# Kernel tuning notes

Measured on AMD Instinct MI355X. Metric: run time of the kernel, lower is better.

The kernel has to match this reference:

```python
import jax, jax.numpy as jnp
import numpy as np

N = 100000   # total nodes
E = 500000   # directed edges
G = 100      # graphs in batch (1000 nodes each)
D = 146      # in/hidden/out dim
C = 10       # classes
BN_EPS = 1e-5


def setup_inputs():
    key = jax.random.key(0)
    ks = jax.random.split(key, 20)
    nodes_feat = jax.random.normal(ks[0], (N, D), jnp.float32)
    src = jax.random.randint(ks[1], (E,), 0, N, dtype=jnp.int32)
    dst = jax.random.randint(ks[2], (E,), 0, N, dtype=jnp.int32)
    graph_ids = (jnp.arange(N, dtype=jnp.int32) // (N // G)).astype(jnp.int32)
    snorm = jnp.full((N,), 1.0 / np.sqrt(N // G), jnp.float32)
    s = 0.05
    W_emb = jax.random.normal(ks[3], (D, D), jnp.float32) * s
    b_emb = jnp.zeros((D,), jnp.float32)
    Ws = jax.random.normal(ks[4], (4, D, D), jnp.float32) * s
    bs = jnp.zeros((4, D), jnp.float32)
    gammas = jnp.ones((4, D), jnp.float32)
    betas = jnp.zeros((4, D), jnp.float32)
    W1 = jax.random.normal(ks[5], (D, D // 2), jnp.float32) * s
    b1 = jnp.zeros((D // 2,), jnp.float32)
    W2 = jax.random.normal(ks[6], (D // 2, D // 4), jnp.float32) * s
    b2 = jnp.zeros((D // 4,), jnp.float32)
    W3 = jax.random.normal(ks[7], (D // 4, C), jnp.float32) * s
    b3 = jnp.zeros((C,), jnp.float32)
    return dict(nodes_feat=nodes_feat, snorm=snorm, W_emb=W_emb, b_emb=b_emb,
                Ws=Ws, bs=bs, gammas=gammas, betas=betas,
                W1=W1, b1=b1, W2=W2, b2=b2, W3=W3, b3=b3,
                src=src, dst=dst, graph_ids=graph_ids)


def _gcn_layer(h, W, b, gamma, beta, src, dst, norm_out, norm_in, snorm):
    h_in = h
    # GraphConv norm='both': D_out^{-1/2} on source, sum-aggregate, D_in^{-1/2} on dest
    m = (h * norm_out[:, None])[src]                     # [E, D] gather
    agg = jax.ops.segment_sum(m, dst, num_segments=N)    # [N, D] scatter-add
    h = agg * norm_in[:, None] @ W + b                   # linear
    h = h * snorm[:, None]                               # graph norm
    mu = jnp.mean(h, axis=0)
    var = jnp.var(h, axis=0)
    h = (h - mu) * jax.lax.rsqrt(var + BN_EPS) * gamma + beta  # batch norm
    h = jax.nn.relu(h)
    return h_in + h                                      # residual


def reference(nodes_feat, snorm, W_emb, b_emb, Ws, bs, gammas, betas,
              W1, b1, W2, b2, W3, b3, src, dst, graph_ids):
    ones_e = jnp.ones((E,), jnp.float32)
    deg_out = jnp.clip(jax.ops.segment_sum(ones_e, src, num_segments=N), 1.0)
    deg_in = jnp.clip(jax.ops.segment_sum(ones_e, dst, num_segments=N), 1.0)
    norm_out = jax.lax.rsqrt(deg_out)
    norm_in = jax.lax.rsqrt(deg_in)

    h = nodes_feat @ W_emb + b_emb                       # embedding_h
    for i in range(4):
        h = _gcn_layer(h, Ws[i], bs[i], gammas[i], betas[i],
                       src, dst, norm_out, norm_in, snorm)

    # mean_nodes per graph
    cnt = jax.ops.segment_sum(jnp.ones((N,), jnp.float32), graph_ids, num_segments=G)
    hg = jax.ops.segment_sum(h, graph_ids, num_segments=G) / cnt[:, None]

    # MLPReadout: 146 -> 73 -> 36 -> 10
    x = jax.nn.relu(hg @ W1 + b1)
    x = jax.nn.relu(x @ W2 + b2)
    return x @ W3 + b3
```

## Files before the change

### kernel.cpp

```cpp
#include <hip/hip_runtime.h>

#define N_NODES 100000
#define N_EDGES 500000
#define N_GRAPHS 100
#define DIM 146
#define APAD 160
#define TPW 160
#define BN_EPS 1e-5f
#define GS_PART 8
#define GS_STRIDE 147
#define ST_PART 4

typedef __bf16 bf16x8 __attribute__((ext_vector_type(8)));
typedef float floatx4 __attribute__((ext_vector_type(4)));
typedef unsigned short ushort_t;
typedef unsigned int uint_t;

__device__ inline ushort_t f2bf(float x) {
  uint_t u = __float_as_uint(x);
  uint_t r = (u + 0x7fffu + ((u >> 16) & 1u)) >> 16;
  return (ushort_t)r;
}
__device__ inline float bf2f(ushort_t b) { return __uint_as_float((uint_t)b << 16); }
__device__ inline uint_t pack2bf(float a, float b) {
  return (uint_t)f2bf(a) | ((uint_t)f2bf(b) << 16);
}
__device__ inline float bflo(uint_t u) { return __uint_as_float(u << 16); }
__device__ inline float bfhi(uint_t u) { return __uint_as_float(u & 0xffff0000u); }

__device__ inline void async_cp16(const ushort_t* g, ushort_t* l) {
  __builtin_amdgcn_global_load_lds((const __attribute__((address_space(1))) void*)g,
                                   (__attribute__((address_space(3))) void*)l, 16, 0, 0);
}

__global__ void hist_kernel(const int* __restrict__ src, const int* __restrict__ dst,
                            int* __restrict__ deg_out, int* __restrict__ deg_in) {
  int e = blockIdx.x * 256 + threadIdx.x;
  if (e < N_EDGES) {
    atomicAdd(&deg_out[src[e]], 1);
    atomicAdd(&deg_in[dst[e]], 1);
  }
}

__global__ void norm_kernel(const int* __restrict__ deg_out, const int* __restrict__ deg_in,
                            float* __restrict__ norm_out, float* __restrict__ norm_in) {
  int v = blockIdx.x * 256 + threadIdx.x;
  if (v < N_NODES) {
    norm_out[v] = rsqrtf((float)max(deg_out[v], 1));
    norm_in[v]  = rsqrtf((float)max(deg_in[v], 1));
  }
}

__global__ void scan1_kernel(const int* __restrict__ deg_in, int* __restrict__ bsums) {
  __shared__ int sred[256];
  int t0 = blockIdx.x * 1024 + threadIdx.x * 4;
  int s = 0;
#pragma unroll
  for (int i = 0; i < 4; i++) { int v = t0 + i; s += (v < N_NODES) ? deg_in[v] : 0; }
  sred[threadIdx.x] = s; __syncthreads();
  for (int off = 128; off > 0; off >>= 1) {
    if (threadIdx.x < off) sred[threadIdx.x] += sred[threadIdx.x + off];
    __syncthreads();
  }
  if (threadIdx.x == 0) bsums[blockIdx.x] = sred[0];
}

__global__ void scan2_kernel(const int* __restrict__ bsums, int* __restrict__ bofs,
                             int* __restrict__ row_ptr, int nb) {
  if (threadIdx.x == 0 && blockIdx.x == 0) {
    int run = 0;
    for (int i = 0; i < nb; i++) { bofs[i] = run; run += bsums[i]; }
    row_ptr[N_NODES] = run;
  }
}

__global__ void scan3_kernel(const int* __restrict__ deg_in, const int* __restrict__ bofs,
                             int* __restrict__ row_ptr) {
  __shared__ int ssc[256];
  int t0 = blockIdx.x * 1024 + threadIdx.x * 4;
  int v4[4]; int s = 0;
#pragma unroll
  for (int i = 0; i < 4; i++) { int v = t0 + i; v4[i] = (v < N_NODES) ? deg_in[v] : 0; s += v4[i]; }
  ssc[threadIdx.x] = s; __syncthreads();
  for (int off = 1; off < 256; off <<= 1) {
    int t = (threadIdx.x >= off) ? ssc[threadIdx.x - off] : 0;
    __syncthreads();
    ssc[threadIdx.x] += t;
    __syncthreads();
  }
  int ex = ssc[threadIdx.x] - s + bofs[blockIdx.x];
#pragma unroll
  for (int i = 0; i < 4; i++) {
    int v = t0 + i;
    if (v < N_NODES) { row_ptr[v] = ex; ex += v4[i]; }
  }
}

__global__ void csr_fill_kernel(const int* __restrict__ src, const int* __restrict__ dst,
                                const int* __restrict__ row_ptr, int* __restrict__ fill,
                                int* __restrict__ csr) {
  int e = blockIdx.x * 256 + threadIdx.x;
  if (e < N_EDGES) {
    int d = dst[e];
    int slot = atomicAdd(&fill[d], 1);
    csr[row_ptr[d] + slot] = src[e];
  }
}

__global__ void wtrans_kernel(const float* __restrict__ W_emb, const float* __restrict__ Ws,
                              ushort_t* __restrict__ Wh) {
  int idx = blockIdx.x * 256 + threadIdx.x;
  if (idx >= 5 * 5 * 10 * 64 * 8) return;
  int j = idx & 7;
  int t = idx >> 3;
  int lane = t & 63; t >>= 6;
  int nt = t % 10; t /= 10;
  int kc = t % 5;
  int m = t / 5;
  const float* W = (m == 0) ? W_emb : Ws + (size_t)(m - 1) * DIM * DIM;
  int k = kc * 32 + (lane >> 4) * 8 + j;
  int n = nt * 16 + (lane & 15);
  float w = (k < DIM && n < DIM) ? W[k * DIM + n] : 0.f;
  Wh[(size_t)(((m * 5 + kc) * 10 + nt) * 64 + lane) * 8 + j] = f2bf(w);
}

__device__ inline bf16x8 make_frag(const float* __restrict__ nf, int row, int kc, int quad) {
  union { bf16x8 v; ushort_t u[8]; } r;
  const float* p = nf + (size_t)row * DIM + kc * 32 + quad * 8;
  int c0 = kc * 32 + quad * 8;
  if (c0 + 8 <= DIM) {
    float2 q0 = *(const float2*)(p);
    float2 q1 = *(const float2*)(p + 2);
    float2 q2 = *(const float2*)(p + 4);
    float2 q3 = *(const float2*)(p + 6);
    r.u[0] = f2bf(q0.x); r.u[1] = f2bf(q0.y); r.u[2] = f2bf(q1.x); r.u[3] = f2bf(q1.y);
    r.u[4] = f2bf(q2.x); r.u[5] = f2bf(q2.y); r.u[6] = f2bf(q3.x); r.u[7] = f2bf(q3.y);
  } else {
#pragma unroll
    for (int j = 0; j < 8; j++) r.u[j] = (c0 + j < DIM) ? f2bf(p[j]) : (ushort_t)0;
  }
  return r.v;
}

__global__ __launch_bounds__(512, 4) void gemm_embed_kernel(
    const float* __restrict__ nf, const ushort_t* __restrict__ Wh,
    const float* __restrict__ bias, ushort_t* __restrict__ hbf) {
  __shared__ __align__(16) ushort_t sW[25600];
  int wave = threadIdx.x >> 6, lane = threadIdx.x & 63;
  int quad = lane >> 4, l16 = lane & 15;
  int m0 = blockIdx.x * 256 + wave * 32;
  int ra = min(m0 + l16, N_NODES - 1);
  int rb = min(m0 + 16 + l16, N_NODES - 1);

#pragma unroll
  for (int i = 0; i < 7; i++) {
    int idx = threadIdx.x + i * 512;
    if (idx < 3200) async_cp16(Wh + idx * 8, sW + idx * 8);
  }
  __syncthreads();

  floatx4 acc[2][10];
#pragma unroll
  for (int s = 0; s < 2; s++)
#pragma unroll
    for (int nt = 0; nt < 10; nt++) acc[s][nt] = (floatx4){0.f, 0.f, 0.f, 0.f};

#pragma unroll 1
  for (int kc = 0; kc < 5; kc++) {
    bf16x8 a0 = make_frag(nf, ra, kc, quad);
    bf16x8 a1 = make_frag(nf, rb, kc, quad);
    const ushort_t* bp = &sW[kc * 5120 + lane * 8];
#pragma unroll
    for (int nt = 0; nt < 10; nt++) {
      bf16x8 bh = *(const bf16x8*)(bp + nt * 512);
      acc[0][nt] = __builtin_amdgcn_mfma_f32_16x16x32_bf16(a0, bh, acc[0][nt], 0, 0, 0);
      acc[1][nt] = __builtin_amdgcn_mfma_f32_16x16x32_bf16(a1, bh, acc[1][nt], 0, 0, 0);
    }
  }

#pragma unroll
  for (int nt = 0; nt < 10; nt++) {
    int c = nt * 16 + l16;
    float b = (c < DIM) ? bias[c] : 0.f;
#pragma unroll
    for (int s = 0; s < 2; s++)
#pragma unroll
      for (int r = 0; r < 4; r++) {
        int row = m0 + s * 16 + quad * 4 + r;
        hbf[(size_t)row * APAD + c] = f2bf(acc[s][nt][r] + b);
      }
  }
}

__global__ __launch_bounds__(512, 4) void gemm_kernel(
    const ushort_t* __restrict__ Abf, const ushort_t* __restrict__ Wh,
    const float* __restrict__ bias, const float* __restrict__ snorm,
    ushort_t* __restrict__ tmpb, float* __restrict__ stats) {
  __shared__ __align__(16) ushort_t sW[25600];
  __shared__ float sred[2 * DIM];
  int wave = threadIdx.x >> 6, lane = threadIdx.x & 63;
  int quad = lane >> 4, l16 = lane & 15;
  int m0 = blockIdx.x * 256 + wave * 32;
  int ra = min(m0 + l16, N_NODES - 1);
  int rb = min(m0 + 16 + l16, N_NODES - 1);
  const ushort_t* ap0 = Abf + (size_t)ra * APAD + quad * 8;
  const ushort_t* ap1 = Abf + (size_t)rb * APAD + quad * 8;

#pragma unroll
  for (int i = 0; i < 7; i++) {
    int idx = threadIdx.x + i * 512;
    if (idx < 3200) async_cp16(Wh + idx * 8, sW + idx * 8);
  }
  bf16x8 na0 = *(const bf16x8*)(ap0);
  bf16x8 na1 = *(const bf16x8*)(ap1);
  for (int i = threadIdx.x; i < 2 * DIM; i += 512) sred[i] = 0.f;
  __syncthreads();

  floatx4 acc[2][10];
#pragma unroll
  for (int s = 0; s < 2; s++)
#pragma unroll
    for (int nt = 0; nt < 10; nt++) acc[s][nt] = (floatx4){0.f, 0.f, 0.f, 0.f};

#pragma unroll 1
  for (int kc = 0; kc < 5; kc++) {
    bf16x8 a0 = na0, a1 = na1;
    if (kc < 4) {
      na0 = *(const bf16x8*)(ap0 + (kc + 1) * 32);
      na1 = *(const bf16x8*)(ap1 + (kc + 1) * 32);
    }
    const ushort_t* bp = &sW[kc * 5120 + lane * 8];
#pragma unroll
    for (int nt = 0; nt < 10; nt++) {
      bf16x8 bh = *(const bf16x8*)(bp + nt * 512);
      acc[0][nt] = __builtin_amdgcn_mfma_f32_16x16x32_bf16(a0, bh, acc[0][nt], 0, 0, 0);
      acc[1][nt] = __builtin_amdgcn_mfma_f32_16x16x32_bf16(a1, bh, acc[1][nt], 0, 0, 0);
    }
  }

  float sn[2][4];
#pragma unroll
  for (int s = 0; s < 2; s++)
#pragma unroll
    for (int r = 0; r < 4; r++) sn[s][r] = snorm[min(m0 + s * 16 + quad * 4 + r, N_NODES - 1)];

#pragma unroll
  for (int nt = 0; nt < 10; nt++) {
    int c = nt * 16 + l16;
    float b = (c < DIM) ? bias[c] : 0.f;
    float ssum = 0.f, ssq = 0.f;
#pragma unroll
    for (int s = 0; s < 2; s++)
#pragma unroll
      for (int r = 0; r < 4; r++) {
        int row = m0 + s * 16 + quad * 4 + r;
        float val = (acc[s][nt][r] + b) * sn[s][r];
        tmpb[(size_t)row * TPW + c] = f2bf(val);
        if (c < DIM && row < N_NODES) { ssum += val; ssq += val * val; }
      }
    if (c < DIM) {
      ssum += __shfl_xor(ssum, 16, 64); ssum += __shfl_xor(ssum, 32, 64);
      ssq  += __shfl_xor(ssq, 16, 64);  ssq  += __shfl_xor(ssq, 32, 64);
      if (quad == 0) {
        atomicAdd(&sred[c], ssum);
        atomicAdd(&sred[DIM + c], ssq);
      }
    }
  }
  __syncthreads();
  float* stp = stats + (blockIdx.x & (ST_PART - 1)) * 2 * DIM;
  for (int i = threadIdx.x; i < 2 * DIM; i += 512) atomicAdd(&stp[i], sred[i]);
}

__global__ __launch_bounds__(256) void agg_kernel(
    const ushort_t* __restrict__ hbf, const int* __restrict__ row_ptr,
    const int* __restrict__ csr, const float* __restrict__ norm_out,
    const float* __restrict__ norm_in, ushort_t* __restrict__ xb) {
  int wid = threadIdx.x >> 6, lane = threadIdx.x & 63;
  int v = blockIdx.x * 4 + wid;
  if (v >= N_NODES) return;
  int e0 = row_ptr[v], e1 = row_ptr[v + 1];
  bool act = lane < 40;
  int col8 = lane * 4;
  float a0 = 0.f, a1 = 0.f, a2 = 0.f, a3 = 0.f;
  float b0 = 0.f, b1 = 0.f, b2 = 0.f, b3 = 0.f;
  float c0 = 0.f, c1 = 0.f, c2 = 0.f, c3 = 0.f;
  float d0 = 0.f, d1 = 0.f, d2 = 0.f, d3 = 0.f;
  int e = e0;
  for (; e + 3 < e1; e += 4) {
    int s0 = csr[e], s1 = csr[e + 1], s2 = csr[e + 2], s3 = csr[e + 3];
    float n0 = norm_out[s0], n1 = norm_out[s1], n2 = norm_out[s2], n3 = norm_out[s3];
    if (act) {
      uint2 u0 = *(const uint2*)(hbf + (size_t)s0 * APAD + col8);
      uint2 u1 = *(const uint2*)(hbf + (size_t)s1 * APAD + col8);
      uint2 u2 = *(const uint2*)(hbf + (size_t)s2 * APAD + col8);
      uint2 u3 = *(const uint2*)(hbf + (size_t)s3 * APAD + col8);
      a0 = fmaf(bflo(u0.x), n0, a0); a1 = fmaf(bfhi(u0.x), n0, a1);
      a2 = fmaf(bflo(u0.y), n0, a2); a3 = fmaf(bfhi(u0.y), n0, a3);
      b0 = fmaf(bflo(u1.x), n1, b0); b1 = fmaf(bfhi(u1.x), n1, b1);
      b2 = fmaf(bflo(u1.y), n1, b2); b3 = fmaf(bfhi(u1.y), n1, b3);
      c0 = fmaf(bflo(u2.x), n2, c0); c1 = fmaf(bfhi(u2.x), n2, c1);
      c2 = fmaf(bflo(u2.y), n2, c2); c3 = fmaf(bfhi(u2.y), n2, c3);
      d0 = fmaf(bflo(u3.x), n3, d0); d1 = fmaf(bfhi(u3.x), n3, d1);
      d2 = fmaf(bflo(u3.y), n3, d2); d3 = fmaf(bfhi(u3.y), n3, d3);
    }
  }
  for (; e < e1; e++) {
    int s0 = csr[e];
    float n0 = norm_out[s0];
    if (act) {
      uint2 u0 = *(const uint2*)(hbf + (size_t)s0 * APAD + col8);
      a0 = fmaf(bflo(u0.x), n0, a0); a1 = fmaf(bfhi(u0.x), n0, a1);
      a2 = fmaf(bflo(u0.y), n0, a2); a3 = fmaf(bfhi(u0.y), n0, a3);
    }
  }
  if (act) {
    float ni = norm_in[v];
    uint2 o;
    o.x = pack2bf((a0 + b0 + c0 + d0) * ni, (a1 + b1 + c1 + d1) * ni);
    o.y = pack2bf((a2 + b2 + c2 + d2) * ni, (a3 + b3 + c3 + d3) * ni);
    *(uint2*)((uint_t*)(xb + (size_t)v * APAD) + lane * 2) = o;
  }
}

__global__ __launch_bounds__(256) void bn_kernel(const ushort_t* __restrict__ tmpb,
                                                 const float* __restrict__ stats,
                                                 const float* __restrict__ gamma,
                                                 const float* __restrict__ beta,
                                                 ushort_t* __restrict__ hbf) {
  __shared__ float2 scs[80], shs[80];
  int t = threadIdx.x;
  if (t < 80) {
    float2 sc = make_float2(0.f, 0.f), sh = make_float2(0.f, 0.f);
    if (t < DIM / 2) {
      int c0 = 2 * t, c1 = c0 + 1;
      float su0 = 0.f, su1 = 0.f, sq0 = 0.f, sq1 = 0.f;
#pragma unroll
      for (int p = 0; p < ST_PART; p++) {
        const float* sp = stats + p * 2 * DIM;
        su0 += sp[c0]; su1 += sp[c1];
        sq0 += sp[DIM + c0]; sq1 += sp[DIM + c1];
      }
      float mu0 = su0 * (1.f / N_NODES), mu1 = su1 * (1.f / N_NODES);
      float v0 = sq0 * (1.f / N_NODES) - mu0 * mu0;
      float v1 = sq1 * (1.f / N_NODES) - mu1 * mu1;
      sc.x = gamma[c0] * rsqrtf(v0 + BN_EPS);
      sc.y = gamma[c1] * rsqrtf(v1 + BN_EPS);
      sh.x = beta[c0] - mu0 * sc.x;
      sh.y = beta[c1] - mu1 * sc.y;
    }
    scs[t] = sc; shs[t] = sh;
  }
  __syncthreads();
  int idx = blockIdx.x * 256 + t;
  if (idx >= N_NODES * 20) return;
  int v = idx / 20, q = idx - v * 20;
  const uint4* tp = (const uint4*)(tmpb + (size_t)v * TPW);
  uint4* hp = (uint4*)(hbf + (size_t)v * APAD);
  uint4 tu = tp[q];
  uint4 hu = hp[q];
  uint4 o;
  {
    float2 sc = scs[q * 4 + 0], sh = shs[q * 4 + 0];
    float x0 = fmaxf(fmaf(bflo(tu.x), sc.x, sh.x), 0.f);
    float x1 = fmaxf(fmaf(bfhi(tu.x), sc.y, sh.y), 0.f);
    o.x = pack2bf(bflo(hu.x) + x0, bfhi(hu.x) + x1);
  }
  {
    float2 sc = scs[q * 4 + 1], sh = shs[q * 4 + 1];
    float x0 = fmaxf(fmaf(bflo(tu.y), sc.x, sh.x), 0.f);
    float x1 = fmaxf(fmaf(bfhi(tu.y), sc.y, sh.y), 0.f);
    o.y = pack2bf(bflo(hu.y) + x0, bfhi(hu.y) + x1);
  }
  {
    float2 sc = scs[q * 4 + 2], sh = shs[q * 4 + 2];
    float x0 = fmaxf(fmaf(bflo(tu.z), sc.x, sh.x), 0.f);
    float x1 = fmaxf(fmaf(bfhi(tu.z), sc.y, sh.y), 0.f);
    o.z = pack2bf(bflo(hu.z) + x0, bfhi(hu.z) + x1);
  }
  {
    float2 sc = scs[q * 4 + 3], sh = shs[q * 4 + 3];
    float x0 = fmaxf(fmaf(bflo(tu.w), sc.x, sh.x), 0.f);
    float x1 = fmaxf(fmaf(bfhi(tu.w), sc.y, sh.y), 0.f);
    o.w = pack2bf(bflo(hu.w) + x0, bfhi(hu.w) + x1);
  }
  hp[q] = o;
}

__global__ __launch_bounds__(192) void gsum_kernel(
    const ushort_t* __restrict__ tmpb, const float* __restrict__ stats,
    const float* __restrict__ gamma, const float* __restrict__ beta,
    const ushort_t* __restrict__ hbf, const int* __restrict__ gids,
    float* __restrict__ hgp) {
  int t = threadIdx.x;
  if (t > DIM) return;
  float sc = 0.f, sh = 0.f;
  if (t < DIM) {
    float su = 0.f, sq = 0.f;
#pragma unroll
    for (int p = 0; p < ST_PART; p++) {
      const float* sp = stats + p * 2 * DIM;
      su += sp[t]; sq += sp[DIM + t];
    }
    float mu = su * (1.f / N_NODES);
    float var = sq * (1.f / N_NODES) - mu * mu;
    sc = gamma[t] * rsqrtf(var + BN_EPS);
    sh = beta[t] - mu * sc;
  }
  int r0 = blockIdx.x * 64;
  int part = blockIdx.x & (GS_PART - 1);
  float accv = 0.f;
  int g_prev = gids[r0];
  for (int rr = 0; rr < 64; rr++) {
    int r = r0 + rr;
    if (r >= N_NODES) break;
    int g = gids[r];
    if (g != g_prev) {
      atomicAdd(&hgp[(size_t)(part * N_GRAPHS + g_prev) * GS_STRIDE + t], accv);
      accv = 0.f; g_prev = g;
    }
    float val;
    if (t < DIM) {
      float x = fmaf(bf2f(tmpb[(size_t)r * TPW + t]), sc, sh);
      x = fmaxf(x, 0.f);
      val = bf2f(hbf[(size_t)r * APAD + t]) + x;
    } else {
      val = 1.f;
    }
    accv += val;
  }
  atomicAdd(&hgp[(size_t)(part * N_GRAPHS + g_prev) * GS_STRIDE + t], accv);
}

__global__ __launch_bounds__(256) void mlp_kernel(
    const float* __restrict__ hgp,
    const float* __restrict__ W1, const float* __restrict__ b1,
    const float* __restrict__ W2, const float* __restrict__ b2,
    const float* __restrict__ W3, const float* __restrict__ b3,
    float* __restrict__ out) {
  __shared__ float hrow[DIM];
  __shared__ float x1[73];
  __shared__ float x2[36];
  int g = blockIdx.x;
  int t = threadIdx.x;
  if (t < DIM) {
    float s = 0.f, cnt = 0.f;
#pragma unroll
    for (int p = 0; p < GS_PART; p++) {
      const float* row = hgp + (size_t)(p * N_GRAPHS + g) * GS_STRIDE;
      s += row[t];
      cnt += row[DIM];
    }
    hrow[t] = s / cnt;
  }
  __syncthreads();
  if (t < 73) {
    float s = b1[t];
    for (int k = 0; k < DIM; k++) s = fmaf(hrow[k], W1[k * 73 + t], s);
    x1[t] = s > 0.f ? s : 0.f;
  }
  __syncthreads();
  if (t < 36) {
    float s = b2[t];
    for (int k = 0; k < 73; k++) s = fmaf(x1[k], W2[k * 36 + t], s);
    x2[t] = s > 0.f ? s : 0.f;
  }
  __syncthreads();
  if (t < 10) {
    float s = b3[t];
    for (int k = 0; k < 36; k++) s = fmaf(x2[k], W3[k * 10 + t], s);
    out[g * 10 + t] = s;
  }
}

extern "C" void kernel_launch(void* const* d_in, const int* in_sizes, int n_in,
                              void* d_out, int out_size, void* d_ws, size_t ws_size,
                              hipStream_t stream) {
  const float* nodes_feat = (const float*)d_in[0];
  const float* snorm  = (const float*)d_in[1];
  const float* W_emb  = (const float*)d_in[2];
  const float* b_emb  = (const float*)d_in[3];
  const float* Ws     = (const float*)d_in[4];
  const float* bs     = (const float*)d_in[5];
  const float* gammas = (const float*)d_in[6];
  const float* betas  = (const float*)d_in[7];
  const float* W1 = (const float*)d_in[8];
  const float* b1 = (const float*)d_in[9];
  const float* W2 = (const float*)d_in[10];
  const float* b2 = (const float*)d_in[11];
  const float* W3 = (const float*)d_in[12];
  const float* b3 = (const float*)d_in[13];
  const int* src  = (const int*)d_in[14];
  const int* dst  = (const int*)d_in[15];
  const int* gids = (const int*)d_in[16];
  float* out = (float*)d_out;

  const int GB = (N_NODES + 255) / 256;
  const int NPADROWS = GB * 256;

  char* base = (char*)d_ws;
  size_t off = 0;
  auto alloc = [&](size_t bytes) { void* p = base + off; off += (bytes + 255) & ~size_t(255); return p; };
  ushort_t* hbf  = (ushort_t*)alloc((size_t)NPADROWS * APAD * 2);
  ushort_t* tmpb = (ushort_t*)alloc((size_t)NPADROWS * TPW * 2);
  ushort_t* xb   = (ushort_t*)alloc((size_t)N_NODES * APAD * 2);
  char* zstart = base + off;
  int* deg_out = (int*)alloc(N_NODES * 4);
  int* deg_in  = (int*)alloc(N_NODES * 4);
  int* fill    = (int*)alloc(N_NODES * 4);
  float* stats = (float*)alloc(4 * ST_PART * 2 * DIM * 4);
  float* hgp   = (float*)alloc((size_t)GS_PART * N_GRAPHS * GS_STRIDE * 4);
  size_t zbytes = (size_t)((base + off) - zstart);
  int* row_ptr = (int*)alloc((N_NODES + 1) * 4);
  float* norm_out = (float*)alloc(N_NODES * 4);
  float* norm_in  = (float*)alloc(N_NODES * 4);
  int* csr   = (int*)alloc((size_t)N_EDGES * 4);
  int* bsums = (int*)alloc(128 * 4);
  int* bofs  = (int*)alloc(128 * 4);
  ushort_t* Wh = (ushort_t*)alloc((size_t)5 * 5 * 10 * 64 * 8 * 2);

  hipMemsetAsync(zstart, 0, zbytes, stream);

  hist_kernel<<<(N_EDGES + 255) / 256, 256, 0, stream>>>(src, dst, deg_out, deg_in);
  norm_kernel<<<(N_NODES + 255) / 256, 256, 0, stream>>>(deg_out, deg_in, norm_out, norm_in);
  int nb = (N_NODES + 1023) / 1024;
  scan1_kernel<<<nb, 256, 0, stream>>>(deg_in, bsums);
  scan2_kernel<<<1, 64, 0, stream>>>(bsums, bofs, row_ptr, nb);
  scan3_kernel<<<nb, 256, 0, stream>>>(deg_in, bofs, row_ptr);
  csr_fill_kernel<<<(N_EDGES + 255) / 256, 256, 0, stream>>>(src, dst, row_ptr, fill, csr);
  wtrans_kernel<<<(5 * 5 * 10 * 64 * 8 + 255) / 256, 256, 0, stream>>>(W_emb, Ws, Wh);

  const size_t WHM = (size_t)5 * 10 * 64 * 8;

  gemm_embed_kernel<<<GB, 512, 0, stream>>>(nodes_feat, Wh, b_emb, hbf);

  for (int l = 0; l < 4; l++) {
    float* st = stats + (size_t)l * ST_PART * 2 * DIM;
    agg_kernel<<<(N_NODES + 3) / 4, 256, 0, stream>>>(hbf, row_ptr, csr, norm_out, norm_in, xb);
    gemm_kernel<<<GB, 512, 0, stream>>>(xb, Wh + (size_t)(l + 1) * WHM, bs + l * DIM,
                                        snorm, tmpb, st);
    if (l < 3) {
      bn_kernel<<<(N_NODES * 20 + 255) / 256, 256, 0, stream>>>(
          tmpb, st, gammas + l * DIM, betas + l * DIM, hbf);
    } else {
      gsum_kernel<<<(N_NODES + 63) / 64, 192, 0, stream>>>(
          tmpb, st, gammas + l * DIM, betas + l * DIM, hbf, gids, hgp);
    }
  }

  mlp_kernel<<<N_GRAPHS, 256, 0, stream>>>(hgp, W1, b1, W2, b2, W3, b3, out);
}
```

Before: 598.9 us.

## Fuse batch norm and residual into GEMM using a grid-wide barrier

The GEMM kernel now keeps its accumulators in registers, computes the batch-norm statistics, and waits at a software grid barrier built from device-scope atomics. After the barrier it reads the global statistics and applies batch norm, ReLU and the residual add straight into hbf. This removes the bf16 tmp buffer round trip and the separate bn kernel launches, and gsum now only sums hbf. The barrier needs all 391 blocks of 512 threads to be resident at once (launch bounds 512,4). If they are not all co-resident it can deadlock, and the spin wait idles every CU until the slowest block finishes.

```diff
diff --git a/kernel.cpp b/kernel.cpp
--- a/kernel.cpp
+++ b/kernel.cpp
@@ -5,7 +5,6 @@
 #define N_GRAPHS 100
 #define DIM 146
 #define APAD 160
-#define TPW 160
 #define BN_EPS 1e-5f
 #define GS_PART 8
 #define GS_STRIDE 147
@@ -195,7 +194,9 @@
 __global__ __launch_bounds__(512, 4) void gemm_kernel(
     const ushort_t* __restrict__ Abf, const ushort_t* __restrict__ Wh,
     const float* __restrict__ bias, const float* __restrict__ snorm,
-    ushort_t* __restrict__ tmpb, float* __restrict__ stats) {
+    const float* __restrict__ gamma, const float* __restrict__ beta,
+    ushort_t* __restrict__ hbf, float* __restrict__ stats,
+    int* __restrict__ bar, int nblocks) {
   __shared__ __align__(16) ushort_t sW[25600];
   __shared__ float sred[2 * DIM];
   int wave = threadIdx.x >> 6, lane = threadIdx.x & 63;
@@ -247,18 +248,19 @@
 #pragma unroll
   for (int nt = 0; nt < 10; nt++) {
     int c = nt * 16 + l16;
-    float b = (c < DIM) ? bias[c] : 0.f;
-    float ssum = 0.f, ssq = 0.f;
-#pragma unroll
-    for (int s = 0; s < 2; s++)
-#pragma unroll
-      for (int r = 0; r < 4; r++) {
-        int row = m0 + s * 16 + quad * 4 + r;
-        float val = (acc[s][nt][r] + b) * sn[s][r];
-        tmpb[(size_t)row * TPW + c] = f2bf(val);
-        if (c < DIM && row < N_NODES) { ssum += val; ssq += val * val; }
-      }
     if (c < DIM) {
+      float b = bias[c];
+      float ssum = 0.f, ssq = 0.f;
+#pragma unroll
+      for (int s = 0; s < 2; s++)
+#pragma unroll
+        for (int r = 0; r < 4; r++) {
+          int row = m0 + s * 16 + quad * 4 + r;
+          if (row < N_NODES) {
+            float val = (acc[s][nt][r] + b) * sn[s][r];
+            ssum += val; ssq += val * val;
+          }
+        }
       ssum += __shfl_xor(ssum, 16, 64); ssum += __shfl_xor(ssum, 32, 64);
       ssq  += __shfl_xor(ssq, 16, 64);  ssq  += __shfl_xor(ssq, 32, 64);
       if (quad == 0) {
@@ -270,6 +272,56 @@
   __syncthreads();
   float* stp = stats + (blockIdx.x & (ST_PART - 1)) * 2 * DIM;
   for (int i = threadIdx.x; i < 2 * DIM; i += 512) atomicAdd(&stp[i], sred[i]);
+  __threadfence();
+
+  __syncthreads();
+  if (threadIdx.x == 0) {
+    int my = __hip_atomic_load(bar + 1, __ATOMIC_RELAXED, __HIP_MEMORY_SCOPE_AGENT);
+    int a = __hip_atomic_fetch_add(bar, 1, __ATOMIC_ACQ_REL, __HIP_MEMORY_SCOPE_AGENT);
+    if (a == nblocks - 1) {
+      __hip_atomic_store(bar, 0, __ATOMIC_RELAXED, __HIP_MEMORY_SCOPE_AGENT);
+      __hip_atomic_fetch_add(bar + 1, 1, __ATOMIC_RELEASE, __HIP_MEMORY_SCOPE_AGENT);
+    } else {
+      while (__hip_atomic_load(bar + 1, __ATOMIC_ACQUIRE, __HIP_MEMORY_SCOPE_AGENT) == my)
+        __builtin_amdgcn_s_sleep(8);
+    }
+  }
+  __syncthreads();
+
+  if (threadIdx.x < DIM) {
+    int c = threadIdx.x;
+    float su = 0.f, sq = 0.f;
+#pragma unroll
+    for (int p = 0; p < ST_PART; p++) {
+      const float* sp = stats + p * 2 * DIM;
+      su += __hip_atomic_load(&sp[c], __ATOMIC_RELAXED, __HIP_MEMORY_SCOPE_AGENT);
+      sq += __hip_atomic_load(&sp[DIM + c], __ATOMIC_RELAXED, __HIP_MEMORY_SCOPE_AGENT);
+    }
+    float mu = su * (1.f / N_NODES);
+    float var = sq * (1.f / N_NODES) - mu * mu;
+    float sc = gamma[c] * rsqrtf(var + BN_EPS);
+    sred[c] = sc;
+    sred[DIM + c] = beta[c] - mu * sc;
+  }
+  __syncthreads();
+
+#pragma unroll
+  for (int nt = 0; nt < 10; nt++) {
+    int c = nt * 16 + l16;
+    float b  = (c < DIM) ? bias[c] : 0.f;
+    float sc = (c < DIM) ? sred[c] : 0.f;
+    float sh = (c < DIM) ? sred[DIM + c] : 0.f;
+#pragma unroll
+    for (int s = 0; s < 2; s++)
+#pragma unroll
+      for (int r = 0; r < 4; r++) {
+        int row = m0 + s * 16 + quad * 4 + r;
+        float val = (acc[s][nt][r] + b) * sn[s][r];
+        float x = fmaxf(fmaf(val, sc, sh), 0.f);
+        size_t idx = (size_t)row * APAD + c;
+        hbf[idx] = f2bf(bf2f(hbf[idx]) + x);
+      }
+  }
 }
 
 __global__ __launch_bounds__(256) void agg_kernel(
@@ -323,90 +375,11 @@
   }
 }
 
-__global__ __launch_bounds__(256) void bn_kernel(const ushort_t* __restrict__ tmpb,
-                                                 const float* __restrict__ stats,
-                                                 const float* __restrict__ gamma,
-                                                 const float* __restrict__ beta,
-                                                 ushort_t* __restrict__ hbf) {
-  __shared__ float2 scs[80], shs[80];
-  int t = threadIdx.x;
-  if (t < 80) {
-    float2 sc = make_float2(0.f, 0.f), sh = make_float2(0.f, 0.f);
-    if (t < DIM / 2) {
-      int c0 = 2 * t, c1 = c0 + 1;
-      float su0 = 0.f, su1 = 0.f, sq0 = 0.f, sq1 = 0.f;
-#pragma unroll
-      for (int p = 0; p < ST_PART; p++) {
-        const float* sp = stats + p * 2 * DIM;
-        su0 += sp[c0]; su1 += sp[c1];
-        sq0 += sp[DIM + c0]; sq1 += sp[DIM + c1];
-      }
-      float mu0 = su0 * (1.f / N_NODES), mu1 = su1 * (1.f / N_NODES);
-      float v0 = sq0 * (1.f / N_NODES) - mu0 * mu0;
-      float v1 = sq1 * (1.f / N_NODES) - mu1 * mu1;
-      sc.x = gamma[c0] * rsqrtf(v0 + BN_EPS);
-      sc.y = gamma[c1] * rsqrtf(v1 + BN_EPS);
-      sh.x = beta[c0] - mu0 * sc.x;
-      sh.y = beta[c1] - mu1 * sc.y;
-    }
-    scs[t] = sc; shs[t] = sh;
-  }
-  __syncthreads();
-  int idx = blockIdx.x * 256 + t;
-  if (idx >= N_NODES * 20) return;
-  int v = idx / 20, q = idx - v * 20;
-  const uint4* tp = (const uint4*)(tmpb + (size_t)v * TPW);
-  uint4* hp = (uint4*)(hbf + (size_t)v * APAD);
-  uint4 tu = tp[q];
-  uint4 hu = hp[q];
-  uint4 o;
-  {
-    float2 sc = scs[q * 4 + 0], sh = shs[q * 4 + 0];
-    float x0 = fmaxf(fmaf(bflo(tu.x), sc.x, sh.x), 0.f);
-    float x1 = fmaxf(fmaf(bfhi(tu.x), sc.y, sh.y), 0.f);
-    o.x = pack2bf(bflo(hu.x) + x0, bfhi(hu.x) + x1);
-  }
-  {
-    float2 sc = scs[q * 4 + 1], sh = shs[q * 4 + 1];
-    float x0 = fmaxf(fmaf(bflo(tu.y), sc.x, sh.x), 0.f);
-    float x1 = fmaxf(fmaf(bfhi(tu.y), sc.y, sh.y), 0.f);
-    o.y = pack2bf(bflo(hu.y) + x0, bfhi(hu.y) + x1);
-  }
-  {
-    float2 sc = scs[q * 4 + 2], sh = shs[q * 4 + 2];
-    float x0 = fmaxf(fmaf(bflo(tu.z), sc.x, sh.x), 0.f);
-    float x1 = fmaxf(fmaf(bfhi(tu.z), sc.y, sh.y), 0.f);
-    o.z = pack2bf(bflo(hu.z) + x0, bfhi(hu.z) + x1);
-  }
-  {
-    float2 sc = scs[q * 4 + 3], sh = shs[q * 4 + 3];
-    float x0 = fmaxf(fmaf(bflo(tu.w), sc.x, sh.x), 0.f);
-    float x1 = fmaxf(fmaf(bfhi(tu.w), sc.y, sh.y), 0.f);
-    o.w = pack2bf(bflo(hu.w) + x0, bfhi(hu.w) + x1);
-  }
-  hp[q] = o;
-}
-
 __global__ __launch_bounds__(192) void gsum_kernel(
-    const ushort_t* __restrict__ tmpb, const float* __restrict__ stats,
-    const float* __restrict__ gamma, const float* __restrict__ beta,
     const ushort_t* __restrict__ hbf, const int* __restrict__ gids,
     float* __restrict__ hgp) {
   int t = threadIdx.x;
   if (t > DIM) return;
-  float sc = 0.f, sh = 0.f;
-  if (t < DIM) {
-    float su = 0.f, sq = 0.f;
-#pragma unroll
-    for (int p = 0; p < ST_PART; p++) {
-      const float* sp = stats + p * 2 * DIM;
-      su += sp[t]; sq += sp[DIM + t];
-    }
-    float mu = su * (1.f / N_NODES);
-    float var = sq * (1.f / N_NODES) - mu * mu;
-    sc = gamma[t] * rsqrtf(var + BN_EPS);
-    sh = beta[t] - mu * sc;
-  }
   int r0 = blockIdx.x * 64;
   int part = blockIdx.x & (GS_PART - 1);
   float accv = 0.f;
@@ -419,15 +392,7 @@
       atomicAdd(&hgp[(size_t)(part * N_GRAPHS + g_prev) * GS_STRIDE + t], accv);
       accv = 0.f; g_prev = g;
     }
-    float val;
-    if (t < DIM) {
-      float x = fmaf(bf2f(tmpb[(size_t)r * TPW + t]), sc, sh);
-      x = fmaxf(x, 0.f);
-      val = bf2f(hbf[(size_t)r * APAD + t]) + x;
-    } else {
-      val = 1.f;
-    }
-    accv += val;
+    accv += (t < DIM) ? bf2f(hbf[(size_t)r * APAD + t]) : 1.f;
   }
   atomicAdd(&hgp[(size_t)(part * N_GRAPHS + g_prev) * GS_STRIDE + t], accv);
 }
@@ -502,7 +467,6 @@
   size_t off = 0;
   auto alloc = [&](size_t bytes) { void* p = base + off; off += (bytes + 255) & ~size_t(255); return p; };
   ushort_t* hbf  = (ushort_t*)alloc((size_t)NPADROWS * APAD * 2);
-  ushort_t* tmpb = (ushort_t*)alloc((size_t)NPADROWS * TPW * 2);
   ushort_t* xb   = (ushort_t*)alloc((size_t)N_NODES * APAD * 2);
   char* zstart = base + off;
   int* deg_out = (int*)alloc(N_NODES * 4);
@@ -510,6 +474,7 @@
   int* fill    = (int*)alloc(N_NODES * 4);
   float* stats = (float*)alloc(4 * ST_PART * 2 * DIM * 4);
   float* hgp   = (float*)alloc((size_t)GS_PART * N_GRAPHS * GS_STRIDE * 4);
+  int* gbar    = (int*)alloc(4 * 16 * 4);
   size_t zbytes = (size_t)((base + off) - zstart);
   int* row_ptr = (int*)alloc((N_NODES + 1) * 4);
   float* norm_out = (float*)alloc(N_NODES * 4);
@@ -538,15 +503,10 @@
     float* st = stats + (size_t)l * ST_PART * 2 * DIM;
     agg_kernel<<<(N_NODES + 3) / 4, 256, 0, stream>>>(hbf, row_ptr, csr, norm_out, norm_in, xb);
     gemm_kernel<<<GB, 512, 0, stream>>>(xb, Wh + (size_t)(l + 1) * WHM, bs + l * DIM,
-                                        snorm, tmpb, st);
-    if (l < 3) {
-      bn_kernel<<<(N_NODES * 20 + 255) / 256, 256, 0, stream>>>(
-          tmpb, st, gammas + l * DIM, betas + l * DIM, hbf);
-    } else {
-      gsum_kernel<<<(N_NODES + 63) / 64, 192, 0, stream>>>(
-          tmpb, st, gammas + l * DIM, betas + l * DIM, hbf, gids, hgp);
-    }
-  }
-
+                                        snorm, gammas + l * DIM, betas + l * DIM,
+                                        hbf, st, gbar + l * 16, GB);
+  }
+
+  gsum_kernel<<<(N_NODES + 63) / 64, 192, 0, stream>>>(hbf, gids, hgp);
   mlp_kernel<<<N_GRAPHS, 256, 0, stream>>>(hgp, W1, b1, W2, b2, W3, b3, out);
 }
```

Result: slower. 1.024 ms (+71.0%).
